# Kernel tuning notes

Measured on AMD Instinct MI355X. Metric: run time of the kernel, lower is better.

## Reference

```python
import jax, jax.numpy as jnp
import numpy as np

B, L, D, H = 2, 2048, 1024, 16
DK = D // H
SCALE = DK ** (-0.25)


def setup_inputs() -> dict:
    key = jax.random.key(0)
    ks = jax.random.split(key, 8)
    return {
        "query": jax.random.normal(ks[0], (B, L, D), jnp.float32),
        "key": jax.random.normal(ks[1], (B, L, D), jnp.float32),
        "value": jax.random.normal(ks[2], (B, L, D), jnp.float32),
        "posbias": jax.random.normal(ks[3], (B, H, L, L), jnp.float32) * 0.1,
        "Wq": jax.random.normal(ks[4], (D, D), jnp.float32) / np.sqrt(D),
        "Wk": jax.random.normal(ks[5], (D, D), jnp.float32) / np.sqrt(D),
        "Wv": jax.random.normal(ks[6], (D, D), jnp.float32) / np.sqrt(D),
        "Wo": jax.random.normal(ks[7], (D, D), jnp.float32) / np.sqrt(D),
    }


def reference(query, key, value, posbias, Wq, Wk, Wv, Wo):
    # nn.Linear(x) = x @ W.T ; weights are [out, in]
    # q: [B, H, L, dk]  k: [B, H, L, dk]  v: [B, H, L, dk]
    q = (query @ Wq.T).reshape(B, L, H, DK).transpose(0, 2, 1, 3) * SCALE
    k = (key @ Wk.T).reshape(B, L, H, DK).transpose(0, 2, 1, 3) * SCALE
    v = (value @ Wv.T).reshape(B, L, H, DK).transpose(0, 2, 1, 3)
    scores = jnp.einsum("bhid,bhjd->bhij", q, k) + posbias  # [B,H,L,L]
    attn = jax.nn.softmax(scores, axis=-1)
    out = jnp.einsum("bhij,bhjd->bhid", attn, v)  # [B,H,L,dk]
    out = out.transpose(0, 2, 1, 3).reshape(B, L, D)
    return out @ Wo.T
```

## Files before the change

kernel.cpp:

```cpp
#include <hip/hip_runtime.h>

#define B_  2
#define L_  2048
#define D_  1024
#define H_  16
#define DK_ 64
#define SCALE_ 0.35355339059327373f

typedef _Float16 f16;
typedef __attribute__((ext_vector_type(8))) _Float16 f16x8;
typedef __attribute__((ext_vector_type(4))) _Float16 f16x4;
typedef __attribute__((ext_vector_type(4))) float    f32x4;

#define AS1C(p) ((const __attribute__((address_space(1))) void*)(p))
#define AS3(p)  ((__attribute__((address_space(3))) void*)(p))

__global__ void cvt_f32_f16(const float* __restrict__ in, f16* __restrict__ out, int n) {
    int i = (blockIdx.x * blockDim.x + threadIdx.x) * 4;
    if (i < n) {
        float4 v = *(const float4*)&in[i];
        f16x4 o;
        o[0] = (f16)v.x; o[1] = (f16)v.y; o[2] = (f16)v.z; o[3] = (f16)v.w;
        *(f16x4*)&out[i] = o;
    }
}

template <typename OutT>
__global__ __launch_bounds__(256) void gemm_bt(
    const f16* __restrict__ A, const f16* __restrict__ Bm, OutT* __restrict__ C,
    int M, int N, int Kd, float alpha)
{
    __shared__ f16 As[128 * 32];
    __shared__ f16 Bs[128 * 32];

    const int tid  = threadIdx.x;
    const int lane = tid & 63;
    const int w    = tid >> 6;
    const int quad = lane >> 4;
    const int l16  = lane & 15;
    const int wm   = w & 1, wn = w >> 1;
    const int m0   = blockIdx.y * 128;
    const int n0   = blockIdx.x * 128;

    f32x4 acc[4][4] = {};

    for (int k0 = 0; k0 < Kd; k0 += 32) {
#pragma unroll
        for (int it = 0; it < 2; ++it) {
            int c    = tid + it * 256;
            int row  = c >> 2;
            int koff = (c & 3) * 8;
            __builtin_amdgcn_global_load_lds(AS1C(&A[(size_t)(m0 + row) * Kd + k0 + koff]),
                                             AS3(&As[c * 8]), 16, 0, 0);
            __builtin_amdgcn_global_load_lds(AS1C(&Bm[(size_t)(n0 + row) * Kd + k0 + koff]),
                                             AS3(&Bs[c * 8]), 16, 0, 0);
        }
        __syncthreads();

        f16x8 af[4], bf[4];
#pragma unroll
        for (int i = 0; i < 4; ++i) {
            af[i] = *(const f16x8*)&As[(wm * 64 + i * 16 + l16) * 32 + quad * 8];
            bf[i] = *(const f16x8*)&Bs[(wn * 64 + i * 16 + l16) * 32 + quad * 8];
        }
#pragma unroll
        for (int i = 0; i < 4; ++i)
#pragma unroll
            for (int j = 0; j < 4; ++j)
                acc[i][j] = __builtin_amdgcn_mfma_f32_16x16x32_f16(af[i], bf[j], acc[i][j], 0, 0, 0);
        __syncthreads();
    }

#pragma unroll
    for (int i = 0; i < 4; ++i)
#pragma unroll
        for (int j = 0; j < 4; ++j)
#pragma unroll
            for (int r = 0; r < 4; ++r) {
                int row = m0 + wm * 64 + i * 16 + quad * 4 + r;
                int col = n0 + wn * 64 + j * 16 + l16;
                C[(size_t)row * N + col] = (OutT)(acc[i][j][r] * alpha);
            }
}

__global__ __launch_bounds__(256) void attn_kernel(
    const f16* __restrict__ Q, const f16* __restrict__ K, const f16* __restrict__ V,
    const float* __restrict__ bias, f16* __restrict__ ctx)
{
    const int qt = blockIdx.x & 31;
    const int h  = (blockIdx.x >> 5) & 15;
    const int b  = blockIdx.x >> 9;
    const int q0 = qt * 64;

    const int tid  = threadIdx.x;
    const int w    = tid >> 6;
    const int lane = tid & 63;
    const int quad = lane >> 4;
    const int l16  = lane & 15;

    __shared__ f16 VT[64][72];
    __shared__ f16 P[4][16][72];

    const size_t bh = (size_t)b * L_ * D_ + (size_t)h * DK_;

    f16x8 qf[2];
    {
        const size_t qrow = (size_t)(q0 + w * 16 + l16);
#pragma unroll
        for (int ks = 0; ks < 2; ++ks)
            qf[ks] = *(const f16x8*)&Q[bh + qrow * D_ + ks * 32 + quad * 8];
    }

    f32x4 oacc[4] = {};
    float m_r[4], l_r[4];
#pragma unroll
    for (int r = 0; r < 4; ++r) { m_r[r] = -1e30f; l_r[r] = 0.f; }

    const float* biasrow = bias + ((size_t)(b * H_ + h) * L_ + q0 + w * 16) * L_;

    for (int j0 = 0; j0 < L_; j0 += 64) {
        {
            int r  = tid >> 2;
            int c0 = (tid & 3) * 16;
            f16x8 v0 = *(const f16x8*)&V[bh + (size_t)(j0 + r) * D_ + c0];
            f16x8 v1 = *(const f16x8*)&V[bh + (size_t)(j0 + r) * D_ + c0 + 8];
#pragma unroll
            for (int i = 0; i < 8; ++i) {
                VT[c0 + i][r]     = v0[i];
                VT[c0 + 8 + i][r] = v1[i];
            }
        }

        f32x4 s[4];
#pragma unroll
        for (int g = 0; g < 4; ++g) {
            const size_t krow = (size_t)(j0 + g * 16 + l16);
            f16x8 kf0 = *(const f16x8*)&K[bh + krow * D_ + quad * 8];
            f16x8 kf1 = *(const f16x8*)&K[bh + krow * D_ + 32 + quad * 8];
            f32x4 a = {};
            a = __builtin_amdgcn_mfma_f32_16x16x32_f16(qf[0], kf0, a, 0, 0, 0);
            a = __builtin_amdgcn_mfma_f32_16x16x32_f16(qf[1], kf1, a, 0, 0, 0);
            s[g] = a;
        }

#pragma unroll
        for (int g = 0; g < 4; ++g)
#pragma unroll
            for (int r = 0; r < 4; ++r)
                s[g][r] += biasrow[(size_t)(quad * 4 + r) * L_ + j0 + g * 16 + l16];

        float alpha[4];
#pragma unroll
        for (int r = 0; r < 4; ++r) {
            float mx = fmaxf(fmaxf(s[0][r], s[1][r]), fmaxf(s[2][r], s[3][r]));
#pragma unroll
            for (int off = 1; off < 16; off <<= 1)
                mx = fmaxf(mx, __shfl_xor(mx, off, 64));
            float mi = fmaxf(m_r[r], mx);
            alpha[r] = __expf(m_r[r] - mi);
            m_r[r]   = mi;
        }
#pragma unroll
        for (int g = 0; g < 4; ++g)
#pragma unroll
            for (int r = 0; r < 4; ++r)
                s[g][r] = __expf(s[g][r] - m_r[r]);
#pragma unroll
        for (int r = 0; r < 4; ++r) {
            float sm = s[0][r] + s[1][r] + s[2][r] + s[3][r];
#pragma unroll
            for (int off = 1; off < 16; off <<= 1)
                sm += __shfl_xor(sm, off, 64);
            l_r[r] = l_r[r] * alpha[r] + sm;
        }
#pragma unroll
        for (int g = 0; g < 4; ++g)
#pragma unroll
            for (int r = 0; r < 4; ++r)
                oacc[g][r] *= alpha[r];

#pragma unroll
        for (int g = 0; g < 4; ++g)
#pragma unroll
            for (int r = 0; r < 4; ++r)
                P[w][quad * 4 + r][g * 16 + l16] = (f16)s[g][r];

        __syncthreads();

#pragma unroll
        for (int ks = 0; ks < 2; ++ks) {
            f16x8 pf = *(const f16x8*)&P[w][l16][ks * 32 + quad * 8];
#pragma unroll
            for (int g = 0; g < 4; ++g) {
                f16x8 vf = *(const f16x8*)&VT[g * 16 + l16][ks * 32 + quad * 8];
                oacc[g] = __builtin_amdgcn_mfma_f32_16x16x32_f16(pf, vf, oacc[g], 0, 0, 0);
            }
        }
        __syncthreads();
    }

#pragma unroll
    for (int g = 0; g < 4; ++g)
#pragma unroll
        for (int r = 0; r < 4; ++r) {
            size_t row = (size_t)(q0 + w * 16 + quad * 4 + r);
            ctx[(size_t)b * L_ * D_ + row * D_ + h * DK_ + g * 16 + l16] =
                (f16)(oacc[g][r] / l_r[r]);
        }
}

extern "C" void kernel_launch(void* const* d_in, const int* in_sizes, int n_in,
                              void* d_out, int out_size, void* d_ws, size_t ws_size,
                              hipStream_t stream)
{
    const float* query = (const float*)d_in[0];
    const float* key   = (const float*)d_in[1];
    const float* value = (const float*)d_in[2];
    const float* pbias = (const float*)d_in[3];
    const float* Wq    = (const float*)d_in[4];
    const float* Wk    = (const float*)d_in[5];
    const float* Wv    = (const float*)d_in[6];
    const float* Wo    = (const float*)d_in[7];
    float* out = (float*)d_out;

    char* ws = (char*)d_ws;
    f16* q16  = (f16*)(ws + 0);
    f16* k16  = (f16*)(ws + 8388608);
    f16* v16  = (f16*)(ws + 16777216);
    f16* wq16 = (f16*)(ws + 25165824);
    f16* wk16 = (f16*)(ws + 27262976);
    f16* wv16 = (f16*)(ws + 29360128);
    f16* wo16 = (f16*)(ws + 31457280);
    f16* Qs   = (f16*)(ws + 33554432);
    f16* Ks   = (f16*)(ws + 41943040);
    f16* Vs   = (f16*)(ws + 50331648);
    f16* ctx  = (f16*)(ws + 58720256);

    const int ML = B_ * L_;
    const int nBig = ML * D_;
    const int nW   = D_ * D_;

    cvt_f32_f16<<<dim3((nBig / 4 + 255) / 256), 256, 0, stream>>>(query, q16, nBig);
    cvt_f32_f16<<<dim3((nBig / 4 + 255) / 256), 256, 0, stream>>>(key,   k16, nBig);
    cvt_f32_f16<<<dim3((nBig / 4 + 255) / 256), 256, 0, stream>>>(value, v16, nBig);
    cvt_f32_f16<<<dim3((nW / 4 + 255) / 256), 256, 0, stream>>>(Wq, wq16, nW);
    cvt_f32_f16<<<dim3((nW / 4 + 255) / 256), 256, 0, stream>>>(Wk, wk16, nW);
    cvt_f32_f16<<<dim3((nW / 4 + 255) / 256), 256, 0, stream>>>(Wv, wv16, nW);
    cvt_f32_f16<<<dim3((nW / 4 + 255) / 256), 256, 0, stream>>>(Wo, wo16, nW);

    dim3 gg(D_ / 128, ML / 128);
    gemm_bt<f16><<<gg, 256, 0, stream>>>(q16, wq16, Qs, ML, D_, D_, SCALE_);
    gemm_bt<f16><<<gg, 256, 0, stream>>>(k16, wk16, Ks, ML, D_, D_, SCALE_);
    gemm_bt<f16><<<gg, 256, 0, stream>>>(v16, wv16, Vs, ML, D_, D_, 1.0f);

    attn_kernel<<<dim3(B_ * H_ * (L_ / 64)), 256, 0, stream>>>(Qs, Ks, Vs, pbias, ctx);

    gemm_bt<float><<<gg, 256, 0, stream>>>(ctx, wo16, out, ML, D_, D_, 1.0f);
}
```

Before: 954.2 us.

## Batch conversions and QKV GEMMs, pre-transpose V, drop attention block syncs

```diff
diff --git a/kernel.cpp b/kernel.cpp
--- a/kernel.cpp
+++ b/kernel.cpp
@@ -9,29 +9,34 @@
 
 typedef _Float16 f16;
 typedef __attribute__((ext_vector_type(8))) _Float16 f16x8;
-typedef __attribute__((ext_vector_type(4))) _Float16 f16x4;
 typedef __attribute__((ext_vector_type(4))) float    f32x4;
 
 #define AS1C(p) ((const __attribute__((address_space(1))) void*)(p))
 #define AS3(p)  ((__attribute__((address_space(3))) void*)(p))
 
-__global__ void cvt_f32_f16(const float* __restrict__ in, f16* __restrict__ out, int n) {
-    int i = (blockIdx.x * blockDim.x + threadIdx.x) * 4;
-    if (i < n) {
-        float4 v = *(const float4*)&in[i];
-        f16x4 o;
-        o[0] = (f16)v.x; o[1] = (f16)v.y; o[2] = (f16)v.z; o[3] = (f16)v.w;
-        *(f16x4*)&out[i] = o;
-    }
-}
-
-template <typename OutT>
-__global__ __launch_bounds__(256) void gemm_bt(
+struct CvtArgs { const float* src[7]; f16* dst[7]; int n[7]; };
+
+__global__ __launch_bounds__(256) void cvt_all(CvtArgs a) {
+    const int s = blockIdx.y;
+    const int i = (blockIdx.x * 256 + threadIdx.x) * 8;
+    if (i >= a.n[s]) return;
+    const float4* p = (const float4*)(a.src[s] + i);
+    float4 v0 = p[0], v1 = p[1];
+    f16x8 o;
+    o[0] = (f16)v0.x; o[1] = (f16)v0.y; o[2] = (f16)v0.z; o[3] = (f16)v0.w;
+    o[4] = (f16)v1.x; o[5] = (f16)v1.y; o[6] = (f16)v1.z; o[7] = (f16)v1.w;
+    *(f16x8*)(a.dst[s] + i) = o;
+}
+
+template <int BM, int BN, typename OutT>
+__device__ __forceinline__ void gemm_core(
     const f16* __restrict__ A, const f16* __restrict__ Bm, OutT* __restrict__ C,
-    int M, int N, int Kd, float alpha)
-{
-    __shared__ f16 As[128 * 32];
-    __shared__ f16 Bs[128 * 32];
+    int N, int Kd, float alpha, int m0, int n0)
+{
+    constexpr int FM = BM / 32;
+    constexpr int FN = BN / 32;
+    __shared__ f16 As[BM * 32];
+    __shared__ f16 Bs[BN * 32];
 
     const int tid  = threadIdx.x;
     const int lane = tid & 63;
@@ -39,52 +44,103 @@
     const int quad = lane >> 4;
     const int l16  = lane & 15;
     const int wm   = w & 1, wn = w >> 1;
-    const int m0   = blockIdx.y * 128;
-    const int n0   = blockIdx.x * 128;
-
-    f32x4 acc[4][4] = {};
+
+    f32x4 acc[FM][FN] = {};
+
+    constexpr int ACH = BM * 4;
+    constexpr int TCH = (BM + BN) * 4;
 
     for (int k0 = 0; k0 < Kd; k0 += 32) {
 #pragma unroll
-        for (int it = 0; it < 2; ++it) {
-            int c    = tid + it * 256;
-            int row  = c >> 2;
-            int koff = (c & 3) * 8;
-            __builtin_amdgcn_global_load_lds(AS1C(&A[(size_t)(m0 + row) * Kd + k0 + koff]),
-                                             AS3(&As[c * 8]), 16, 0, 0);
-            __builtin_amdgcn_global_load_lds(AS1C(&Bm[(size_t)(n0 + row) * Kd + k0 + koff]),
-                                             AS3(&Bs[c * 8]), 16, 0, 0);
+        for (int c = tid; c < TCH; c += 256) {
+            if (c < ACH) {
+                int row = c >> 2, koff = (c & 3) * 8;
+                __builtin_amdgcn_global_load_lds(AS1C(&A[(size_t)(m0 + row) * Kd + k0 + koff]),
+                                                 AS3(&As[c * 8]), 16, 0, 0);
+            } else {
+                int c2 = c - ACH;
+                int row = c2 >> 2, koff = (c2 & 3) * 8;
+                __builtin_amdgcn_global_load_lds(AS1C(&Bm[(size_t)(n0 + row) * Kd + k0 + koff]),
+                                                 AS3(&Bs[c2 * 8]), 16, 0, 0);
+            }
         }
         __syncthreads();
 
-        f16x8 af[4], bf[4];
-#pragma unroll
-        for (int i = 0; i < 4; ++i) {
-            af[i] = *(const f16x8*)&As[(wm * 64 + i * 16 + l16) * 32 + quad * 8];
-            bf[i] = *(const f16x8*)&Bs[(wn * 64 + i * 16 + l16) * 32 + quad * 8];
-        }
-#pragma unroll
-        for (int i = 0; i < 4; ++i)
-#pragma unroll
-            for (int j = 0; j < 4; ++j)
+        f16x8 af[FM], bf[FN];
+#pragma unroll
+        for (int i = 0; i < FM; ++i)
+            af[i] = *(const f16x8*)&As[(wm * (BM / 2) + i * 16 + l16) * 32 + quad * 8];
+#pragma unroll
+        for (int j = 0; j < FN; ++j)
+            bf[j] = *(const f16x8*)&Bs[(wn * (BN / 2) + j * 16 + l16) * 32 + quad * 8];
+#pragma unroll
+        for (int i = 0; i < FM; ++i)
+#pragma unroll
+            for (int j = 0; j < FN; ++j)
                 acc[i][j] = __builtin_amdgcn_mfma_f32_16x16x32_f16(af[i], bf[j], acc[i][j], 0, 0, 0);
         __syncthreads();
     }
 
 #pragma unroll
-    for (int i = 0; i < 4; ++i)
-#pragma unroll
-        for (int j = 0; j < 4; ++j)
+    for (int i = 0; i < FM; ++i)
+#pragma unroll
+        for (int j = 0; j < FN; ++j)
 #pragma unroll
             for (int r = 0; r < 4; ++r) {
-                int row = m0 + wm * 64 + i * 16 + quad * 4 + r;
-                int col = n0 + wn * 64 + j * 16 + l16;
+                int row = m0 + wm * (BM / 2) + i * 16 + quad * 4 + r;
+                int col = n0 + wn * (BN / 2) + j * 16 + l16;
                 C[(size_t)row * N + col] = (OutT)(acc[i][j][r] * alpha);
             }
 }
 
+struct G3 { const f16* A[3]; const f16* W[3]; f16* O[3]; float alpha[3]; };
+
+__global__ __launch_bounds__(256) void gemm3_qkv(G3 g, int M, int N, int Kd) {
+    const int z = blockIdx.z;
+    gemm_core<128, 128, f16>(g.A[z], g.W[z], g.O[z], N, Kd, g.alpha[z],
+                             blockIdx.y * 128, blockIdx.x * 128);
+}
+
+__global__ __launch_bounds__(256) void gemm_wo(
+    const f16* __restrict__ A, const f16* __restrict__ W, float* __restrict__ C,
+    int M, int N, int Kd)
+{
+    gemm_core<128, 64, float>(A, W, C, N, Kd, 1.0f, blockIdx.y * 128, blockIdx.x * 64);
+}
+
+__global__ __launch_bounds__(256) void transpose_v(
+    const f16* __restrict__ Vs, f16* __restrict__ VT)
+{
+    const int jt = blockIdx.x & 31;
+    const int h  = (blockIdx.x >> 5) & 15;
+    const int b  = blockIdx.x >> 9;
+    const int j0 = jt * 64;
+
+    __shared__ f16 T[64][72];
+
+    const int t   = threadIdx.x;
+    const int tok = t >> 2;
+    const int c0  = (t & 3) * 16;
+
+    const f16* src = Vs + (size_t)b * L_ * D_ + (size_t)(j0 + tok) * D_ + h * DK_ + c0;
+    f16x8 v0 = *(const f16x8*)src;
+    f16x8 v1 = *(const f16x8*)(src + 8);
+#pragma unroll
+    for (int i = 0; i < 8; ++i) {
+        T[c0 + i][tok]     = v0[i];
+        T[c0 + 8 + i][tok] = v1[i];
+    }
+    __syncthreads();
+
+    const int dk = t >> 2;
+    const int jj = (t & 3) * 16;
+    f16* dst = VT + ((size_t)(b * H_ + h) * DK_ + dk) * L_ + j0 + jj;
+    *(f16x8*)dst       = *(const f16x8*)&T[dk][jj];
+    *(f16x8*)(dst + 8) = *(const f16x8*)&T[dk][jj + 8];
+}
+
 __global__ __launch_bounds__(256) void attn_kernel(
-    const f16* __restrict__ Q, const f16* __restrict__ K, const f16* __restrict__ V,
+    const f16* __restrict__ Q, const f16* __restrict__ K, const f16* __restrict__ VT,
     const float* __restrict__ bias, f16* __restrict__ ctx)
 {
     const int qt = blockIdx.x & 31;
@@ -98,10 +154,10 @@
     const int quad = lane >> 4;
     const int l16  = lane & 15;
 
-    __shared__ f16 VT[64][72];
     __shared__ f16 P[4][16][72];
 
-    const size_t bh = (size_t)b * L_ * D_ + (size_t)h * DK_;
+    const size_t bh  = (size_t)b * L_ * D_ + (size_t)h * DK_;
+    const size_t bhv = (size_t)(b * H_ + h) * DK_ * L_;
 
     f16x8 qf[2];
     {
@@ -119,18 +175,6 @@
     const float* biasrow = bias + ((size_t)(b * H_ + h) * L_ + q0 + w * 16) * L_;
 
     for (int j0 = 0; j0 < L_; j0 += 64) {
-        {
-            int r  = tid >> 2;
-            int c0 = (tid & 3) * 16;
-            f16x8 v0 = *(const f16x8*)&V[bh + (size_t)(j0 + r) * D_ + c0];
-            f16x8 v1 = *(const f16x8*)&V[bh + (size_t)(j0 + r) * D_ + c0 + 8];
-#pragma unroll
-            for (int i = 0; i < 8; ++i) {
-                VT[c0 + i][r]     = v0[i];
-                VT[c0 + 8 + i][r] = v1[i];
-            }
-        }
-
         f32x4 s[4];
 #pragma unroll
         for (int g = 0; g < 4; ++g) {
@@ -185,18 +229,16 @@
             for (int r = 0; r < 4; ++r)
                 P[w][quad * 4 + r][g * 16 + l16] = (f16)s[g][r];
 
-        __syncthreads();
-
 #pragma unroll
         for (int ks = 0; ks < 2; ++ks) {
             f16x8 pf = *(const f16x8*)&P[w][l16][ks * 32 + quad * 8];
 #pragma unroll
             for (int g = 0; g < 4; ++g) {
-                f16x8 vf = *(const f16x8*)&VT[g * 16 + l16][ks * 32 + quad * 8];
+                f16x8 vf = *(const f16x8*)&VT[bhv + (size_t)(g * 16 + l16) * L_ +
+                                              j0 + ks * 32 + quad * 8];
                 oacc[g] = __builtin_amdgcn_mfma_f32_16x16x32_f16(pf, vf, oacc[g], 0, 0, 0);
             }
         }
-        __syncthreads();
     }
 
 #pragma unroll
@@ -224,36 +266,43 @@
     float* out = (float*)d_out;
 
     char* ws = (char*)d_ws;
-    f16* q16  = (f16*)(ws + 0);
-    f16* k16  = (f16*)(ws + 8388608);
-    f16* v16  = (f16*)(ws + 16777216);
-    f16* wq16 = (f16*)(ws + 25165824);
-    f16* wk16 = (f16*)(ws + 27262976);
-    f16* wv16 = (f16*)(ws + 29360128);
-    f16* wo16 = (f16*)(ws + 31457280);
-    f16* Qs   = (f16*)(ws + 33554432);
-    f16* Ks   = (f16*)(ws + 41943040);
-    f16* Vs   = (f16*)(ws + 50331648);
-    f16* ctx  = (f16*)(ws + 58720256);
-
-    const int ML = B_ * L_;
+    const size_t MB = 1024 * 1024;
+    f16* q16  = (f16*)(ws + 0 * MB);
+    f16* k16  = (f16*)(ws + 8 * MB);
+    f16* v16  = (f16*)(ws + 16 * MB);
+    f16* wq16 = (f16*)(ws + 24 * MB);
+    f16* wk16 = (f16*)(ws + 26 * MB);
+    f16* wv16 = (f16*)(ws + 28 * MB);
+    f16* wo16 = (f16*)(ws + 30 * MB);
+    f16* Qs   = (f16*)(ws + 32 * MB);
+    f16* Ks   = (f16*)(ws + 40 * MB);
+    f16* Vs   = (f16*)(ws + 48 * MB);
+    f16* VTg  = (f16*)(ws + 56 * MB);
+    f16* ctx  = (f16*)(ws + 64 * MB);
+
+    const int ML   = B_ * L_;
     const int nBig = ML * D_;
     const int nW   = D_ * D_;
 
-    cvt_f32_f16<<<dim3((nBig / 4 + 255) / 256), 256, 0, stream>>>(query, q16, nBig);
-    cvt_f32_f16<<<dim3((nBig / 4 + 255) / 256), 256, 0, stream>>>(key,   k16, nBig);
-    cvt_f32_f16<<<dim3((nBig / 4 + 255) / 256), 256, 0, stream>>>(value, v16, nBig);
-    cvt_f32_f16<<<dim3((nW / 4 + 255) / 256), 256, 0, stream>>>(Wq, wq16, nW);
-    cvt_f32_f16<<<dim3((nW / 4 + 255) / 256), 256, 0, stream>>>(Wk, wk16, nW);
-    cvt_f32_f16<<<dim3((nW / 4 + 255) / 256), 256, 0, stream>>>(Wv, wv16, nW);
-    cvt_f32_f16<<<dim3((nW / 4 + 255) / 256), 256, 0, stream>>>(Wo, wo16, nW);
-
-    dim3 gg(D_ / 128, ML / 128);
-    gemm_bt<f16><<<gg, 256, 0, stream>>>(q16, wq16, Qs, ML, D_, D_, SCALE_);
-    gemm_bt<f16><<<gg, 256, 0, stream>>>(k16, wk16, Ks, ML, D_, D_, SCALE_);
-    gemm_bt<f16><<<gg, 256, 0, stream>>>(v16, wv16, Vs, ML, D_, D_, 1.0f);
-
-    attn_kernel<<<dim3(B_ * H_ * (L_ / 64)), 256, 0, stream>>>(Qs, Ks, Vs, pbias, ctx);
-
-    gemm_bt<float><<<gg, 256, 0, stream>>>(ctx, wo16, out, ML, D_, D_, 1.0f);
-}
+    CvtArgs ca;
+    ca.src[0] = query; ca.dst[0] = q16;  ca.n[0] = nBig;
+    ca.src[1] = key;   ca.dst[1] = k16;  ca.n[1] = nBig;
+    ca.src[2] = value; ca.dst[2] = v16;  ca.n[2] = nBig;
+    ca.src[3] = Wq;    ca.dst[3] = wq16; ca.n[3] = nW;
+    ca.src[4] = Wk;    ca.dst[4] = wk16; ca.n[4] = nW;
+    ca.src[5] = Wv;    ca.dst[5] = wv16; ca.n[5] = nW;
+    ca.src[6] = Wo;    ca.dst[6] = wo16; ca.n[6] = nW;
+    cvt_all<<<dim3(nBig / (8 * 256), 7), 256, 0, stream>>>(ca);
+
+    G3 g3;
+    g3.A[0] = q16; g3.W[0] = wq16; g3.O[0] = Qs; g3.alpha[0] = SCALE_;
+    g3.A[1] = k16; g3.W[1] = wk16; g3.O[1] = Ks; g3.alpha[1] = SCALE_;
+    g3.A[2] = v16; g3.W[2] = wv16; g3.O[2] = Vs; g3.alpha[2] = 1.0f;
+    gemm3_qkv<<<dim3(D_ / 128, ML / 128, 3), 256, 0, stream>>>(g3, ML, D_, D_);
+
+    transpose_v<<<dim3(B_ * H_ * (L_ / 64)), 256, 0, stream>>>(Vs, VTg);
+
+    attn_kernel<<<dim3(B_ * H_ * (L_ / 64)), 256, 0, stream>>>(Qs, Ks, VTg, pbias, ctx);
+
+    gemm_wo<<<dim3(D_ / 64, ML / 128), 256, 0, stream>>>(ctx, wo16, out, ML, D_, D_);
+}
```

Result: slower. 984.5 us (+3.2%).
